# Performance work log

Hardware: AMD Instinct MI355X
Metric: run time of the kernel (lower is better)

## Reference

```python
import jax, jax.numpy as jnp
import numpy as np

N_NODES = 100000
N_EDGES = 1600000
IN_DIM = 64
HID = 64
EDGE_DIM = 1
NUM_GRAPHS = 1000
SCALE = 0.05


def setup_inputs() -> dict:
    key = jax.random.key(0)
    ks = jax.random.split(key, 20)
    x = jax.random.normal(ks[0], (N_NODES, IN_DIM), dtype=jnp.float32)
    edge_index = jax.random.randint(ks[1], (2, N_EDGES), 0, N_NODES, dtype=jnp.int64)
    edge_attr = jax.random.normal(ks[2], (N_EDGES, EDGE_DIM), dtype=jnp.float32)
    batch = jnp.sort(jax.random.randint(ks[3], (N_NODES,), 0, NUM_GRAPHS, dtype=jnp.int64))
    p = lambda k, shp: SCALE * jax.random.normal(k, shp, dtype=jnp.float32)
    return {
        "x": x, "edge_index": edge_index, "edge_attr": edge_attr, "batch": batch,
        # conv1 MLP + edge lin
        "W1a": p(ks[4], (IN_DIM, HID)), "b1a": p(ks[5], (HID,)),
        "W1b": p(ks[6], (HID, HID)), "b1b": p(ks[7], (HID,)),
        "We1": p(ks[8], (EDGE_DIM, IN_DIM)), "be1": p(ks[9], (IN_DIM,)),
        # conv2 MLP + edge lin
        "W2a": p(ks[10], (HID, HID)), "b2a": p(ks[11], (HID,)),
        "W2b": p(ks[12], (HID, HID)), "b2b": p(ks[13], (HID,)),
        "We2": p(ks[14], (EDGE_DIM, HID)), "be2": p(ks[15], (HID,)),
        # classifier
        "Wc1": p(ks[16], (HID, HID)), "bc1": p(ks[17], (HID,)),
        "Wc2": p(ks[18], (HID, 1)), "bc2": p(ks[19], (1,)),
    }


def _gine(x, src, dst, e_proj, Wa, ba, Wb, bb):
    # message: ReLU(x_src + projected edge feature); scatter-sum to target
    msg = jax.nn.relu(x[src] + e_proj)                      # [E, D]
    agg = jax.ops.segment_sum(msg, dst, num_segments=x.shape[0])
    h = x + agg                                             # eps = 0 (default)
    return jax.nn.relu(h @ Wa + ba) @ Wb + bb               # GIN MLP


def reference(x, edge_index, edge_attr, batch,
              W1a, b1a, W1b, b1b, We1, be1,
              W2a, b2a, W2b, b2b, We2, be2,
              Wc1, bc1, Wc2, bc2):
    src, dst = edge_index[0], edge_index[1]
    h = _gine(x, src, dst, edge_attr @ We1 + be1, W1a, b1a, W1b, b1b)
    h = jax.nn.relu(h)  # dropout is identity in eval mode
    h = _gine(h, src, dst, edge_attr @ We2 + be2, W2a, b2a, W2b, b2b)
    h = jax.nn.relu(h)
    # global mean pool over graphs
    sums = jax.ops.segment_sum(h, batch, num_segments=NUM_GRAPHS)
    cnts = jax.ops.segment_sum(jnp.ones((h.shape[0], 1), h.dtype), batch, num_segments=NUM_GRAPHS)
    pooled = sums / jnp.maximum(cnts, 1.0)                  # [G, HID]
    return jax.nn.relu(pooled @ Wc1 + bc1) @ Wc2 + bc2      # [G, 1]
```

## Files before the change

kernel.cpp:

```cpp
#include <hip/hip_runtime.h>

#define N_NODES    100000
#define N_EDGES    1600000
#define DIM        64
#define NUM_GRAPHS 1000
#define CONV_BLK   3125
#define PAD        72

#define SLICES     512
#define SLICE_E    3125
#define NBUCK      782
#define CAP4       3072

typedef __attribute__((ext_vector_type(8))) short bf16x8;
typedef __attribute__((ext_vector_type(4))) float f32x4;

__device__ __forceinline__ unsigned short f2bf(float f) {
    unsigned int b = __float_as_uint(f);
    b += 0x7FFFu + ((b >> 16) & 1u);
    return (unsigned short)(b >> 16);
}

__device__ __forceinline__ float4 ntload_f4(const float* p) {
    f32x4 v = __builtin_nontemporal_load((const f32x4*)p);
    return make_float4(v.x, v.y, v.z, v.w);
}

__global__ __launch_bounds__(256) void prep(
    const int* __restrict__ ei, const float* __restrict__ x,
    int* __restrict__ hist, int* __restrict__ bucketTotal,
    unsigned short* __restrict__ x16)
{
    __shared__ int lh[NBUCK];
    int blk = blockIdx.x, t = threadIdx.x;
    if (blk < SLICES) {
        for (int i = t; i < NBUCK; i += 256) lh[i] = 0;
        __syncthreads();
        const int* dsts = ei + N_EDGES + blk * SLICE_E;
        for (int k = t; k < SLICE_E; k += 256)
            atomicAdd(&lh[dsts[k] >> 7], 1);
        __syncthreads();
        for (int i = t; i < NBUCK; i += 256) {
            int h = lh[i];
            hist[blk * NBUCK + i] = h;
            if (h) atomicAdd(&bucketTotal[i], h);
        }
    } else {
        int tt = (blk - SLICES) * 256 + t;
        if (tt < N_NODES * DIM / 8) {
            int base = tt * 8;
            float4 f0 = ntload_f4(x + base);
            float4 f1 = ntload_f4(x + base + 4);
            uint4 o;
            o.x = (unsigned)f2bf(f0.x) | ((unsigned)f2bf(f0.y) << 16);
            o.y = (unsigned)f2bf(f0.z) | ((unsigned)f2bf(f0.w) << 16);
            o.z = (unsigned)f2bf(f1.x) | ((unsigned)f2bf(f1.y) << 16);
            o.w = (unsigned)f2bf(f1.z) | ((unsigned)f2bf(f1.w) << 16);
            *(uint4*)(x16 + base) = o;
        }
    }
}

__global__ __launch_bounds__(1024) void csr_c2a(
    const int* __restrict__ bucketTotal, int* __restrict__ bucketStart)
{
    __shared__ int sc[1024];
    int t = threadIdx.x;
    int v = (t < NBUCK) ? bucketTotal[t] : 0;
    sc[t] = v;
    __syncthreads();
    for (int o = 1; o < 1024; o <<= 1) {
        int u = (t >= o) ? sc[t - o] : 0;
        __syncthreads();
        sc[t] += u;
        __syncthreads();
    }
    if (t < NBUCK) bucketStart[t] = sc[t] - v;
    if (t == NBUCK - 1) bucketStart[NBUCK] = sc[t];
}

__global__ __launch_bounds__(512) void csr_c2b(
    const int* __restrict__ hist, const int* __restrict__ bucketStart,
    int* __restrict__ off)
{
    __shared__ int sc[512];
    int b = blockIdx.x, t = threadIdx.x;
    int v = hist[t * NBUCK + b];
    sc[t] = v;
    __syncthreads();
    for (int o = 1; o < 512; o <<= 1) {
        int u = (t >= o) ? sc[t - o] : 0;
        __syncthreads();
        sc[t] += u;
        __syncthreads();
    }
    off[b * SLICES + t] = bucketStart[b] + sc[t] - v;
}

__global__ __launch_bounds__(512) void csr_c3(
    const int* __restrict__ ei, const float* __restrict__ ea,
    const int* __restrict__ hist, const int* __restrict__ off,
    int2* __restrict__ tmp)
{
    __shared__ int2 staging[SLICE_E];
    __shared__ int  lstart[NBUCK + 1];
    __shared__ int  garr[NBUCK];
    __shared__ int  lcur[NBUCK];
    __shared__ unsigned short barr[SLICE_E];
    __shared__ int  part[512];

    int s = blockIdx.x, t = threadIdx.x;

    int h[2];
    int mysum = 0;
    #pragma unroll
    for (int j = 0; j < 2; ++j) {
        int b = 2 * t + j;
        h[j] = (b < NBUCK) ? hist[s * NBUCK + b] : 0;
        mysum += h[j];
    }
    part[t] = mysum;
    for (int i = t; i < NBUCK; i += 512) {
        garr[i] = off[i * SLICES + s];
        lcur[i] = 0;
    }
    __syncthreads();
    for (int o = 1; o < 512; o <<= 1) {
        int u = (t >= o) ? part[t - o] : 0;
        __syncthreads();
        part[t] += u;
        __syncthreads();
    }
    int run = part[t] - mysum;
    #pragma unroll
    for (int j = 0; j < 2; ++j) {
        int b = 2 * t + j;
        if (b < NBUCK) lstart[b] = run;
        run += h[j];
    }
    if (t == 0) lstart[NBUCK] = SLICE_E;
    __syncthreads();

    #pragma unroll
    for (int j = 0; j < 2; ++j) {
        int b = 2 * t + j;
        if (b < NBUCK)
            for (int i = lstart[b]; i < lstart[b + 1]; ++i)
                barr[i] = (unsigned short)b;
    }
    __syncthreads();

    for (int k = t; k < SLICE_E; k += 512) {
        int e   = s * SLICE_E + k;
        int src = ei[e];
        int dst = ei[N_EDGES + e];
        float a = ea[e];
        int b   = dst >> 7;
        int p   = lstart[b] + atomicAdd(&lcur[b], 1);
        staging[p] = make_int2(((dst & 127) << 17) | src, __float_as_int(a));
    }
    __syncthreads();

    for (int i = t; i < SLICE_E; i += 512) {
        int b = barr[i];
        tmp[garr[b] + (i - lstart[b])] = staging[i];
    }
}

__global__ __launch_bounds__(512, 6) void gine_sort(
    const uint2* __restrict__ g2,
    const float* __restrict__ self32,
    const int*   __restrict__ bucketStart,
    const int2*  __restrict__ tmp,
    int2* __restrict__ csr_e,
    int*  __restrict__ rowptr,
    const float* __restrict__ We, const float* __restrict__ be,
    const float* __restrict__ Wa, const float* __restrict__ ba,
    const float* __restrict__ Wb, const float* __restrict__ bb,
    unsigned int* __restrict__ out16)
{
    __shared__ int2 staging[CAP4];
    __shared__ int  nh[128];
    __shared__ int  nscan[128];
    __shared__ int  ncur[128];
    __shared__ short sWat[64 * PAD];
    __shared__ short sWbt[64 * PAD];
    __shared__ short h16[32 * PAD];
    __shared__ short t16[32 * PAD];

    int t = threadIdx.x;
    int b = blockIdx.x;
    int lo = bucketStart[b], hi = bucketStart[b + 1];
    int cnt = hi - lo;
    int node0 = b << 7;
    int nn = min(128, N_NODES - node0);

    for (int i = t; i < 4096; i += 512) {
        int k = i >> 6, n = i & 63;
        sWat[n * PAD + k] = (short)f2bf(Wa[i]);
        sWbt[n * PAD + k] = (short)f2bf(Wb[i]);
    }
    if (t < 128) { nh[t] = 0; ncur[t] = 0; }
    __syncthreads();

    int2 r[6];
    int nr = 0;
    for (int k = t; k < cnt; k += 512) {
        int2 v = tmp[lo + k];
        r[nr++] = v;
        atomicAdd(&nh[v.x >> 17], 1);
    }
    __syncthreads();

    if (t < 128) nscan[t] = nh[t];
    __syncthreads();
    for (int o = 1; o < 128; o <<= 1) {
        int u = (t >= o && t < 128) ? nscan[t - o] : 0;
        __syncthreads();
        if (t < 128) nscan[t] += u;
        __syncthreads();
    }
    if (t < 128) nscan[t] -= nh[t];
    __syncthreads();

    if (t < nn) rowptr[node0 + t] = lo + nscan[t];
    if (b == NBUCK - 1 && t == 0) rowptr[N_NODES] = N_EDGES;

    for (int k = 0; k < nr; ++k) {
        int dl = r[k].x >> 17;
        int p  = nscan[dl] + atomicAdd(&ncur[dl], 1);
        staging[p] = r[k];
    }
    __syncthreads();

    for (int i = t; i < cnt; i += 512) {
        int2 v = staging[i];
        csr_e[lo + i] = make_int2((v.x & 0x1FFFF) << 4, v.y);
    }

    int wave = t >> 6;
    int lane = t & 63;
    int quad = lane >> 4;
    int l15  = lane & 15;
    int slot = wave * 4 + quad;
    int d0   = l15 * 4;
    float4 wp = *(const float4*)(We + d0);
    float4 bp = *(const float4*)(be + d0);
    int mtile = wave & 1;
    int ntile = wave >> 1;
    int col   = ntile * 16 + l15;
    int am    = mtile * 16 + l15;
    float bav = ba[col], bbv = bb[col];
    int cclamp = max(cnt - 1, 0);
    __syncthreads();

    for (int g = 0; g < 4; ++g) {
        int  lrow  = g * 32 + slot;
        bool valid = lrow < nn;
        int deg = valid ? nh[lrow] : 0;
        int beg = valid ? min(nscan[lrow], cclamp) : 0;
        int dm = deg;
        dm = max(dm, __shfl_xor(dm, 16));
        dm = max(dm, __shfl_xor(dm, 32));

        float4 agg = make_float4(0.f, 0.f, 0.f, 0.f);
        #define EDGE4(rr, uu, cond)                                              \
        {                                                                        \
            float s = (cond) ? 1.f : 0.f, av = __int_as_float(rr.y);             \
            float e0 = __uint_as_float(uu.x << 16);                              \
            float e1 = __uint_as_float(uu.x & 0xFFFF0000u);                      \
            float e2 = __uint_as_float(uu.y << 16);                              \
            float e3 = __uint_as_float(uu.y & 0xFFFF0000u);                      \
            agg.x = fmaf(s, fmaxf(e0 + fmaf(av, wp.x, bp.x), 0.f), agg.x);       \
            agg.y = fmaf(s, fmaxf(e1 + fmaf(av, wp.y, bp.y), 0.f), agg.y);       \
            agg.z = fmaf(s, fmaxf(e2 + fmaf(av, wp.z, bp.z), 0.f), agg.z);       \
            agg.w = fmaf(s, fmaxf(e3 + fmaf(av, wp.w, bp.w), 0.f), agg.w);       \
        }
        for (int j = 0; j < dm; j += 4) {
            int2 r0 = staging[beg + ((j + 0) < deg ? j + 0 : 0)];
            int2 r1 = staging[beg + ((j + 1) < deg ? j + 1 : 0)];
            int2 r2 = staging[beg + ((j + 2) < deg ? j + 2 : 0)];
            int2 r3 = staging[beg + ((j + 3) < deg ? j + 3 : 0)];
            uint2 u0 = g2[(r0.x & 0x1FFFF) * 16 + l15];
            uint2 u1 = g2[(r1.x & 0x1FFFF) * 16 + l15];
            uint2 u2 = g2[(r2.x & 0x1FFFF) * 16 + l15];
            uint2 u3 = g2[(r3.x & 0x1FFFF) * 16 + l15];
            EDGE4(r0, u0, (j + 0) < deg)
            EDGE4(r1, u1, (j + 1) < deg)
            EDGE4(r2, u2, (j + 2) < deg)
            EDGE4(r3, u3, (j + 3) < deg)
        }
        #undef EDGE4
        if (valid) {
            float4 sv = *(const float4*)(self32 + (size_t)(node0 + lrow) * DIM + d0);
            agg.x += sv.x; agg.y += sv.y; agg.z += sv.z; agg.w += sv.w;
        }
        {
            unsigned lov = (unsigned)f2bf(agg.x) | ((unsigned)f2bf(agg.y) << 16);
            unsigned hiv = (unsigned)f2bf(agg.z) | ((unsigned)f2bf(agg.w) << 16);
            *(uint2*)&h16[slot * PAD + d0] = make_uint2(lov, hiv);
        }
        __syncthreads();

        f32x4 acc = {bav, bav, bav, bav};
        #pragma unroll
        for (int s = 0; s < 2; ++s) {
            bf16x8 a = *(const bf16x8*)&h16[am * PAD + s * 32 + quad * 8];
            bf16x8 bb8 = *(const bf16x8*)&sWat[col * PAD + s * 32 + quad * 8];
            acc = __builtin_amdgcn_mfma_f32_16x16x32_bf16(a, bb8, acc, 0, 0, 0);
        }
        #pragma unroll
        for (int rr = 0; rr < 4; ++rr) {
            int row = mtile * 16 + quad * 4 + rr;
            t16[row * PAD + col] = (short)f2bf(fmaxf(acc[rr], 0.f));
        }
        __syncthreads();

        f32x4 acc2 = {bbv, bbv, bbv, bbv};
        #pragma unroll
        for (int s = 0; s < 2; ++s) {
            bf16x8 a = *(const bf16x8*)&t16[am * PAD + s * 32 + quad * 8];
            bf16x8 bb8 = *(const bf16x8*)&sWbt[col * PAD + s * 32 + quad * 8];
            acc2 = __builtin_amdgcn_mfma_f32_16x16x32_bf16(a, bb8, acc2, 0, 0, 0);
        }
        #pragma unroll
        for (int rr = 0; rr < 4; ++rr) {
            int row = mtile * 16 + quad * 4 + rr;
            h16[row * PAD + col] = (short)f2bf(fmaxf(acc2[rr], 0.f));
        }
        __syncthreads();
        {
            int n2 = t >> 4, dd = (t & 15) * 2;
            int lnode = g * 32 + n2;
            if (node0 + lnode < N_NODES) {
                uint2 v = *(const uint2*)&h16[n2 * PAD + dd * 2];
                *(uint2*)&out16[(size_t)(node0 + lnode) * 32 + dd] = v;
            }
        }
        __syncthreads();
    }
}

template<bool SELF32>
__global__ __launch_bounds__(512, 8) void gine_mfma(
    const uint2* __restrict__ g2,
    const float* __restrict__ self32,
    const int*   __restrict__ rowptr,
    const int2*  __restrict__ csr_e,
    const float* __restrict__ We, const float* __restrict__ be,
    const float* __restrict__ Wa, const float* __restrict__ ba,
    const float* __restrict__ Wb, const float* __restrict__ bb,
    unsigned int* __restrict__ out16)
{
    __shared__ short sWat[64 * PAD];
    __shared__ short sWbt[64 * PAD];
    __shared__ short h16[32 * PAD];
    __shared__ short t16[32 * PAD];

    int t = threadIdx.x;
    for (int i = t; i < 4096; i += 512) {
        int k = i >> 6, n = i & 63;
        sWat[n * PAD + k] = (short)f2bf(Wa[i]);
        sWbt[n * PAD + k] = (short)f2bf(Wb[i]);
    }
    int wave = t >> 6;
    int lane = t & 63;
    int quad = lane >> 4;
    int l15  = lane & 15;
    int slot = wave * 4 + quad;
    int d0   = l15 * 4;
    float4 wp = *(const float4*)(We + d0);
    float4 bp = *(const float4*)(be + d0);
    int mtile = wave & 1;
    int ntile = wave >> 1;
    int col   = ntile * 16 + l15;
    int am    = mtile * 16 + l15;
    float bav = ba[col], bbv = bb[col];
    __syncthreads();

    for (int base = blockIdx.x * 32; base < N_NODES; base += gridDim.x * 32) {
        int  node  = base + slot;
        bool valid = node < N_NODES;
        int beg = 0, deg = 0;
        if (valid) {
            beg = rowptr[node];
            deg = rowptr[node + 1] - beg;
            beg = min(beg, N_EDGES - 1);
        }
        int dm = deg;
        dm = max(dm, __shfl_xor(dm, 16));
        dm = max(dm, __shfl_xor(dm, 32));

        float4 agg = make_float4(0.f, 0.f, 0.f, 0.f);
        #define EDGE4(rr, uu, cond)                                              \
        {                                                                        \
            float s = (cond) ? 1.f : 0.f, av = __int_as_float(rr.y);             \
            float e0 = __uint_as_float(uu.x << 16);                              \
            float e1 = __uint_as_float(uu.x & 0xFFFF0000u);                      \
            float e2 = __uint_as_float(uu.y << 16);                              \
            float e3 = __uint_as_float(uu.y & 0xFFFF0000u);                      \
            agg.x = fmaf(s, fmaxf(e0 + fmaf(av, wp.x, bp.x), 0.f), agg.x);       \
            agg.y = fmaf(s, fmaxf(e1 + fmaf(av, wp.y, bp.y), 0.f), agg.y);       \
            agg.z = fmaf(s, fmaxf(e2 + fmaf(av, wp.z, bp.z), 0.f), agg.z);       \
            agg.w = fmaf(s, fmaxf(e3 + fmaf(av, wp.w, bp.w), 0.f), agg.w);       \
        }
        for (int j = 0; j < dm; j += 4) {
            int2 r0 = csr_e[beg + ((j + 0) < deg ? j + 0 : 0)];
            int2 r1 = csr_e[beg + ((j + 1) < deg ? j + 1 : 0)];
            int2 r2 = csr_e[beg + ((j + 2) < deg ? j + 2 : 0)];
            int2 r3 = csr_e[beg + ((j + 3) < deg ? j + 3 : 0)];
            uint2 u0 = g2[r0.x + l15];
            uint2 u1 = g2[r1.x + l15];
            uint2 u2 = g2[r2.x + l15];
            uint2 u3 = g2[r3.x + l15];
            EDGE4(r0, u0, (j + 0) < deg)
            EDGE4(r1, u1, (j + 1) < deg)
            EDGE4(r2, u2, (j + 2) < deg)
            EDGE4(r3, u3, (j + 3) < deg)
        }
        #undef EDGE4
        if (valid) {
            if (SELF32) {
                float4 sv = *(const float4*)(self32 + (size_t)node * DIM + d0);
                agg.x += sv.x; agg.y += sv.y; agg.z += sv.z; agg.w += sv.w;
            } else {
                uint2 u = g2[node * 16 + l15];
                agg.x += __uint_as_float(u.x << 16);
                agg.y += __uint_as_float(u.x & 0xFFFF0000u);
                agg.z += __uint_as_float(u.y << 16);
                agg.w += __uint_as_float(u.y & 0xFFFF0000u);
            }
        }
        {
            unsigned lo = (unsigned)f2bf(agg.x) | ((unsigned)f2bf(agg.y) << 16);
            unsigned hi = (unsigned)f2bf(agg.z) | ((unsigned)f2bf(agg.w) << 16);
            *(uint2*)&h16[slot * PAD + d0] = make_uint2(lo, hi);
        }
        __syncthreads();

        f32x4 acc = {bav, bav, bav, bav};
        #pragma unroll
        for (int s = 0; s < 2; ++s) {
            bf16x8 a = *(const bf16x8*)&h16[am * PAD + s * 32 + quad * 8];
            bf16x8 b = *(const bf16x8*)&sWat[col * PAD + s * 32 + quad * 8];
            acc = __builtin_amdgcn_mfma_f32_16x16x32_bf16(a, b, acc, 0, 0, 0);
        }
        #pragma unroll
        for (int r = 0; r < 4; ++r) {
            int row = mtile * 16 + quad * 4 + r;
            t16[row * PAD + col] = (short)f2bf(fmaxf(acc[r], 0.f));
        }
        __syncthreads();

        f32x4 acc2 = {bbv, bbv, bbv, bbv};
        #pragma unroll
        for (int s = 0; s < 2; ++s) {
            bf16x8 a = *(const bf16x8*)&t16[am * PAD + s * 32 + quad * 8];
            bf16x8 b = *(const bf16x8*)&sWbt[col * PAD + s * 32 + quad * 8];
            acc2 = __builtin_amdgcn_mfma_f32_16x16x32_bf16(a, b, acc2, 0, 0, 0);
        }
        #pragma unroll
        for (int r = 0; r < 4; ++r) {
            int row = mtile * 16 + quad * 4 + r;
            h16[row * PAD + col] = (short)f2bf(fmaxf(acc2[r], 0.f));
        }
        __syncthreads();
        {
            int nn = t >> 4, dd = (t & 15) * 2;
            if (base + nn < N_NODES) {
                uint2 v = *(const uint2*)&h16[nn * PAD + dd * 2];
                *(uint2*)&out16[(size_t)(base + nn) * 32 + dd] = v;
            }
        }
        __syncthreads();
    }
}

__device__ __forceinline__ int lbound(const int* __restrict__ a, int key) {
    int lo = 0, hi = N_NODES;
    while (lo < hi) {
        int mid = (lo + hi) >> 1;
        if (a[mid] < key) lo = mid + 1; else hi = mid;
    }
    return lo;
}

__global__ __launch_bounds__(256) void pool_cls(
    const unsigned int* __restrict__ B16b,
    const int* __restrict__ batch,
    const float* __restrict__ Wc1,  const float* __restrict__ bc1,
    const float* __restrict__ Wc2,  const float* __restrict__ bc2,
    float* __restrict__ out)
{
    __shared__ float sW[64 * 64];
    __shared__ float sp[4][64];

    int t = threadIdx.x;
    for (int i = t; i < 64 * 64; i += 256) sW[i] = Wc1[i];

    int nl   = t >> 6;
    int lane = t & 63;
    int g    = blockIdx.x * 4 + nl;

    int p = lane & 31, h = lane >> 5;
    if (g < NUM_GRAPHS) {
        int s = lbound(batch, g);
        int e = lbound(batch, g + 1);
        float2 sum = make_float2(0.f, 0.f);
        for (int i = s + h; i < e; i += 2) {
            unsigned u = B16b[(size_t)i * 32 + p];
            sum.x += __uint_as_float(u << 16);
            sum.y += __uint_as_float(u & 0xFFFF0000u);
        }
        sum.x += __shfl_xor(sum.x, 32);
        sum.y += __shfl_xor(sum.y, 32);
        if (h == 0) {
            float inv = 1.f / (float)max(e - s, 1);
            sp[nl][2 * p]     = sum.x * inv;
            sp[nl][2 * p + 1] = sum.y * inv;
        }
    } else if (h == 0) {
        sp[nl][2 * p] = 0.f;
        sp[nl][2 * p + 1] = 0.f;
    }
    __syncthreads();

    float acc = bc1[lane];
    #pragma unroll
    for (int k = 0; k < 64; ++k)
        acc = fmaf(sp[nl][k], sW[k * 64 + lane], acc);
    float tv = fmaxf(acc, 0.f) * Wc2[lane];

    #pragma unroll
    for (int off = 32; off > 0; off >>= 1)
        tv += __shfl_down(tv, off);

    if (lane == 0 && g < NUM_GRAPHS) out[g] = tv + bc2[0];
}

extern "C" void kernel_launch(void* const* d_in, const int* in_sizes, int n_in,
                              void* d_out, int out_size, void* d_ws, size_t ws_size,
                              hipStream_t stream) {
    const float* x     = (const float*)d_in[0];
    const int*   ei    = (const int*)  d_in[1];
    const float* ea    = (const float*)d_in[2];
    const int*   batch = (const int*)  d_in[3];
    const float* W1a = (const float*)d_in[4];
    const float* b1a = (const float*)d_in[5];
    const float* W1b = (const float*)d_in[6];
    const float* b1b = (const float*)d_in[7];
    const float* We1 = (const float*)d_in[8];
    const float* be1 = (const float*)d_in[9];
    const float* W2a = (const float*)d_in[10];
    const float* b2a = (const float*)d_in[11];
    const float* W2b = (const float*)d_in[12];
    const float* b2b = (const float*)d_in[13];
    const float* We2 = (const float*)d_in[14];
    const float* be2 = (const float*)d_in[15];
    const float* Wc1 = (const float*)d_in[16];
    const float* bc1 = (const float*)d_in[17];
    const float* Wc2 = (const float*)d_in[18];
    const float* bc2 = (const float*)d_in[19];

    int2*           csr_e  = (int2*)d_ws;
    unsigned short* x16    = (unsigned short*)(csr_e + N_EDGES);
    unsigned short* B16    = x16 + (size_t)N_NODES * DIM;
    unsigned short* B16b   = B16 + (size_t)N_NODES * DIM;
    int2*           tmp    = (int2*)B16b;
    int*            hist   = (int*)(B16b + (size_t)N_NODES * DIM);
    int*            off    = hist + SLICES * NBUCK;
    int*            bucketTotal = off + NBUCK * SLICES;
    int*            bucketStart = bucketTotal + NBUCK;
    int*            rowptr = bucketStart + (NBUCK + 1);

    hipMemsetAsync(bucketTotal, 0, NBUCK * sizeof(int), stream);

    prep<<<SLICES + CONV_BLK, 256, 0, stream>>>(ei, x, hist, bucketTotal, x16);
    csr_c2a<<<1, 1024, 0, stream>>>(bucketTotal, bucketStart);
    csr_c2b<<<NBUCK, 512, 0, stream>>>(hist, bucketStart, off);
    csr_c3<<<SLICES, 512, 0, stream>>>(ei, ea, hist, off, tmp);

    gine_sort<<<NBUCK, 512, 0, stream>>>(
        (const uint2*)x16, x, bucketStart, tmp, csr_e, rowptr,
        We1, be1, W1a, b1a, W1b, b1b, (unsigned int*)B16);

    gine_mfma<false><<<1024, 512, 0, stream>>>(
        (const uint2*)B16, nullptr, rowptr, csr_e,
        We2, be2, W2a, b2a, W2b, b2b, (unsigned int*)B16b);

    pool_cls<<<(NUM_GRAPHS + 3) / 4, 256, 0, stream>>>(
        (const unsigned int*)B16b, batch, Wc1, bc1, Wc2, bc2, (float*)d_out);
}
```

Before: 296.5 us.

## Replace per-slice offset scan with atomic bucket cursors and fuse bf16 cast into build

Removes the per-slice histogram array and the column-scan kernel. Each slice block now recomputes its local histogram and reserves its spot in each bucket with an atomicAdd on a global cursor. The x-to-bf16 conversion moves into the build kernel, and the global histogram pass uses fewer, larger blocks. This cuts one kernel launch and the hist/off global traffic, at the cost of reading the destination array twice and making the edge order within a bucket depend on atomic timing.

Measured after the change: 316.4 us. 1.07x slower.

```diff
diff --git a/kernel.cpp b/kernel.cpp
--- a/kernel.cpp
+++ b/kernel.cpp
@@ -4,13 +4,13 @@
 #define N_EDGES    1600000
 #define DIM        64
 #define NUM_GRAPHS 1000
-#define CONV_BLK   3125
 #define PAD        72
 
 #define SLICES     512
 #define SLICE_E    3125
 #define NBUCK      782
 #define CAP4       3072
+#define HIST_BLK   256
 
 typedef __attribute__((ext_vector_type(8))) short bf16x8;
 typedef __attribute__((ext_vector_type(4))) float f32x4;
@@ -26,29 +26,71 @@
     return make_float4(v.x, v.y, v.z, v.w);
 }
 
-__global__ __launch_bounds__(256) void prep(
-    const int* __restrict__ ei, const float* __restrict__ x,
-    int* __restrict__ hist, int* __restrict__ bucketTotal,
-    unsigned short* __restrict__ x16)
+__global__ __launch_bounds__(256) void prep_hist(
+    const int* __restrict__ ei, int* __restrict__ bucketTotal)
 {
     __shared__ int lh[NBUCK];
     int blk = blockIdx.x, t = threadIdx.x;
-    if (blk < SLICES) {
-        for (int i = t; i < NBUCK; i += 256) lh[i] = 0;
-        __syncthreads();
-        const int* dsts = ei + N_EDGES + blk * SLICE_E;
-        for (int k = t; k < SLICE_E; k += 256)
-            atomicAdd(&lh[dsts[k] >> 7], 1);
-        __syncthreads();
-        for (int i = t; i < NBUCK; i += 256) {
-            int h = lh[i];
-            hist[blk * NBUCK + i] = h;
-            if (h) atomicAdd(&bucketTotal[i], h);
-        }
-    } else {
-        int tt = (blk - SLICES) * 256 + t;
-        if (tt < N_NODES * DIM / 8) {
-            int base = tt * 8;
+    for (int i = t; i < NBUCK; i += 256) lh[i] = 0;
+    __syncthreads();
+    const int* dsts = ei + N_EDGES + blk * (2 * SLICE_E);
+    for (int k = t; k < 2 * SLICE_E; k += 256)
+        atomicAdd(&lh[dsts[k] >> 7], 1);
+    __syncthreads();
+    for (int i = t; i < NBUCK; i += 256) {
+        int h = lh[i];
+        if (h) atomicAdd(&bucketTotal[i], h);
+    }
+}
+
+__global__ __launch_bounds__(1024) void csr_c2a(
+    const int* __restrict__ bucketTotal, int* __restrict__ bucketStart,
+    int* __restrict__ cursor)
+{
+    __shared__ int sc[1024];
+    int t = threadIdx.x;
+    int v = (t < NBUCK) ? bucketTotal[t] : 0;
+    sc[t] = v;
+    __syncthreads();
+    for (int o = 1; o < 1024; o <<= 1) {
+        int u = (t >= o) ? sc[t - o] : 0;
+        __syncthreads();
+        sc[t] += u;
+        __syncthreads();
+    }
+    if (t < NBUCK) {
+        int e = sc[t] - v;
+        bucketStart[t] = e;
+        cursor[t] = e;
+    }
+    if (t == NBUCK - 1) bucketStart[NBUCK] = sc[t];
+}
+
+__global__ __launch_bounds__(512) void csr_build(
+    const int* __restrict__ ei, const float* __restrict__ ea,
+    const float* __restrict__ x,
+    int* __restrict__ cursor, int2* __restrict__ tmp,
+    unsigned short* __restrict__ x16)
+{
+    __shared__ int2 staging[SLICE_E];
+    __shared__ int  lh[NBUCK];
+    __shared__ int  lstart[NBUCK + 1];
+    __shared__ int  garr[NBUCK];
+    __shared__ unsigned short barr[SLICE_E];
+    __shared__ int  part[512];
+
+    int s = blockIdx.x, t = threadIdx.x;
+    const int* dsts = ei + N_EDGES + s * SLICE_E;
+
+    for (int i = t; i < NBUCK; i += 512) lh[i] = 0;
+    __syncthreads();
+    for (int k = t; k < SLICE_E; k += 512)
+        atomicAdd(&lh[dsts[k] >> 7], 1);
+
+    {
+        int gid = s * 512 + t;
+        for (int it = gid; it < N_NODES * DIM / 8; it += SLICES * 512) {
+            int base = it * 8;
             float4 f0 = ntload_f4(x + base);
             float4 f1 = ntload_f4(x + base + 4);
             uint4 o;
@@ -59,71 +101,17 @@
             *(uint4*)(x16 + base) = o;
         }
     }
-}
-
-__global__ __launch_bounds__(1024) void csr_c2a(
-    const int* __restrict__ bucketTotal, int* __restrict__ bucketStart)
-{
-    __shared__ int sc[1024];
-    int t = threadIdx.x;
-    int v = (t < NBUCK) ? bucketTotal[t] : 0;
-    sc[t] = v;
-    __syncthreads();
-    for (int o = 1; o < 1024; o <<= 1) {
-        int u = (t >= o) ? sc[t - o] : 0;
-        __syncthreads();
-        sc[t] += u;
-        __syncthreads();
-    }
-    if (t < NBUCK) bucketStart[t] = sc[t] - v;
-    if (t == NBUCK - 1) bucketStart[NBUCK] = sc[t];
-}
-
-__global__ __launch_bounds__(512) void csr_c2b(
-    const int* __restrict__ hist, const int* __restrict__ bucketStart,
-    int* __restrict__ off)
-{
-    __shared__ int sc[512];
-    int b = blockIdx.x, t = threadIdx.x;
-    int v = hist[t * NBUCK + b];
-    sc[t] = v;
-    __syncthreads();
-    for (int o = 1; o < 512; o <<= 1) {
-        int u = (t >= o) ? sc[t - o] : 0;
-        __syncthreads();
-        sc[t] += u;
-        __syncthreads();
-    }
-    off[b * SLICES + t] = bucketStart[b] + sc[t] - v;
-}
-
-__global__ __launch_bounds__(512) void csr_c3(
-    const int* __restrict__ ei, const float* __restrict__ ea,
-    const int* __restrict__ hist, const int* __restrict__ off,
-    int2* __restrict__ tmp)
-{
-    __shared__ int2 staging[SLICE_E];
-    __shared__ int  lstart[NBUCK + 1];
-    __shared__ int  garr[NBUCK];
-    __shared__ int  lcur[NBUCK];
-    __shared__ unsigned short barr[SLICE_E];
-    __shared__ int  part[512];
-
-    int s = blockIdx.x, t = threadIdx.x;
+    __syncthreads();
 
     int h[2];
     int mysum = 0;
     #pragma unroll
     for (int j = 0; j < 2; ++j) {
         int b = 2 * t + j;
-        h[j] = (b < NBUCK) ? hist[s * NBUCK + b] : 0;
+        h[j] = (b < NBUCK) ? lh[b] : 0;
         mysum += h[j];
     }
     part[t] = mysum;
-    for (int i = t; i < NBUCK; i += 512) {
-        garr[i] = off[i * SLICES + s];
-        lcur[i] = 0;
-    }
     __syncthreads();
     for (int o = 1; o < 512; o <<= 1) {
         int u = (t >= o) ? part[t - o] : 0;
@@ -135,12 +123,16 @@
     #pragma unroll
     for (int j = 0; j < 2; ++j) {
         int b = 2 * t + j;
-        if (b < NBUCK) lstart[b] = run;
+        if (b < NBUCK) {
+            lstart[b] = run;
+            if (h[j]) garr[b] = atomicAdd(&cursor[b], h[j]);
+        }
         run += h[j];
     }
     if (t == 0) lstart[NBUCK] = SLICE_E;
     __syncthreads();
 
+    for (int i = t; i < NBUCK; i += 512) lh[i] = 0;
     #pragma unroll
     for (int j = 0; j < 2; ++j) {
         int b = 2 * t + j;
@@ -153,10 +145,10 @@
     for (int k = t; k < SLICE_E; k += 512) {
         int e   = s * SLICE_E + k;
         int src = ei[e];
-        int dst = ei[N_EDGES + e];
+        int dst = dsts[k];
         float a = ea[e];
         int b   = dst >> 7;
-        int p   = lstart[b] + atomicAdd(&lcur[b], 1);
+        int p   = lstart[b] + atomicAdd(&lh[b], 1);
         staging[p] = make_int2(((dst & 127) << 17) | src, __float_as_int(a));
     }
     __syncthreads();
@@ -567,18 +559,16 @@
     unsigned short* B16    = x16 + (size_t)N_NODES * DIM;
     unsigned short* B16b   = B16 + (size_t)N_NODES * DIM;
     int2*           tmp    = (int2*)B16b;
-    int*            hist   = (int*)(B16b + (size_t)N_NODES * DIM);
-    int*            off    = hist + SLICES * NBUCK;
-    int*            bucketTotal = off + NBUCK * SLICES;
+    int*            bucketTotal = (int*)(B16b + (size_t)N_NODES * DIM);
     int*            bucketStart = bucketTotal + NBUCK;
-    int*            rowptr = bucketStart + (NBUCK + 1);
+    int*            cursor = bucketStart + (NBUCK + 1);
+    int*            rowptr = cursor + NBUCK;
 
     hipMemsetAsync(bucketTotal, 0, NBUCK * sizeof(int), stream);
 
-    prep<<<SLICES + CONV_BLK, 256, 0, stream>>>(ei, x, hist, bucketTotal, x16);
-    csr_c2a<<<1, 1024, 0, stream>>>(bucketTotal, bucketStart);
-    csr_c2b<<<NBUCK, 512, 0, stream>>>(hist, bucketStart, off);
-    csr_c3<<<SLICES, 512, 0, stream>>>(ei, ea, hist, off, tmp);
+    prep_hist<<<HIST_BLK, 256, 0, stream>>>(ei, bucketTotal);
+    csr_c2a<<<1, 1024, 0, stream>>>(bucketTotal, bucketStart, cursor);
+    csr_build<<<SLICES, 512, 0, stream>>>(ei, ea, x, cursor, tmp, x16);
 
     gine_sort<<<NBUCK, 512, 0, stream>>>(
         (const uint2*)x16, x, bucketStart, tmp, csr_e, rowptr,
```

## Batch eight buckets per offset-scan block and split conv2 into two half launches

Applied to the files above, without the earlier changes.

The per-bucket offset scan kernel now processes eight buckets per block with a padded shared array, cutting the block count roughly eightfold and amortising the barrier-heavy scan. The second GINE convolution is split into two launches of 512 blocks, each covering half the node range. This may improve cache locality of the gathered rows or load balance, but it adds an extra launch. The unused fp32 self-term template path is removed.

New measurement: 326.2 us. 10.0% more time.

```diff
diff --git a/kernel.cpp b/kernel.cpp
--- a/kernel.cpp
+++ b/kernel.cpp
@@ -6,6 +6,7 @@
 #define NUM_GRAPHS 1000
 #define CONV_BLK   3125
 #define PAD        72
+#define NHALF      50016
 
 #define SLICES     512
 #define SLICE_E    3125
@@ -79,22 +80,36 @@
     if (t == NBUCK - 1) bucketStart[NBUCK] = sc[t];
 }
 
-__global__ __launch_bounds__(512) void csr_c2b(
+__global__ __launch_bounds__(512) void csr_c2b8(
     const int* __restrict__ hist, const int* __restrict__ bucketStart,
     int* __restrict__ off)
 {
-    __shared__ int sc[512];
-    int b = blockIdx.x, t = threadIdx.x;
-    int v = hist[t * NBUCK + b];
-    sc[t] = v;
+    __shared__ int sc[512][9];
+    int blk = blockIdx.x, t = threadIdx.x;
+    int b0 = blk * 8;
+    int v[8];
+    #pragma unroll
+    for (int j = 0; j < 8; ++j) {
+        int b = b0 + j;
+        v[j] = (b < NBUCK) ? hist[t * NBUCK + b] : 0;
+        sc[t][j] = v[j];
+    }
     __syncthreads();
     for (int o = 1; o < 512; o <<= 1) {
-        int u = (t >= o) ? sc[t - o] : 0;
-        __syncthreads();
-        sc[t] += u;
-        __syncthreads();
-    }
-    off[b * SLICES + t] = bucketStart[b] + sc[t] - v;
+        int u[8];
+        #pragma unroll
+        for (int j = 0; j < 8; ++j) u[j] = (t >= o) ? sc[t - o][j] : 0;
+        __syncthreads();
+        #pragma unroll
+        for (int j = 0; j < 8; ++j) sc[t][j] += u[j];
+        __syncthreads();
+    }
+    #pragma unroll
+    for (int j = 0; j < 8; ++j) {
+        int b = b0 + j;
+        if (b < NBUCK)
+            off[b * SLICES + t] = bucketStart[b] + sc[t][j] - v[j];
+    }
 }
 
 __global__ __launch_bounds__(512) void csr_c3(
@@ -341,16 +356,15 @@
     }
 }
 
-template<bool SELF32>
 __global__ __launch_bounds__(512, 8) void gine_mfma(
     const uint2* __restrict__ g2,
-    const float* __restrict__ self32,
     const int*   __restrict__ rowptr,
     const int2*  __restrict__ csr_e,
     const float* __restrict__ We, const float* __restrict__ be,
     const float* __restrict__ Wa, const float* __restrict__ ba,
     const float* __restrict__ Wb, const float* __restrict__ bb,
-    unsigned int* __restrict__ out16)
+    unsigned int* __restrict__ out16,
+    int nbase, int nend)
 {
     __shared__ short sWat[64 * PAD];
     __shared__ short sWbt[64 * PAD];
@@ -378,7 +392,7 @@
     float bav = ba[col], bbv = bb[col];
     __syncthreads();
 
-    for (int base = blockIdx.x * 32; base < N_NODES; base += gridDim.x * 32) {
+    for (int base = nbase + blockIdx.x * 32; base < nend; base += gridDim.x * 32) {
         int  node  = base + slot;
         bool valid = node < N_NODES;
         int beg = 0, deg = 0;
@@ -420,16 +434,11 @@
         }
         #undef EDGE4
         if (valid) {
-            if (SELF32) {
-                float4 sv = *(const float4*)(self32 + (size_t)node * DIM + d0);
-                agg.x += sv.x; agg.y += sv.y; agg.z += sv.z; agg.w += sv.w;
-            } else {
-                uint2 u = g2[node * 16 + l15];
-                agg.x += __uint_as_float(u.x << 16);
-                agg.y += __uint_as_float(u.x & 0xFFFF0000u);
-                agg.z += __uint_as_float(u.y << 16);
-                agg.w += __uint_as_float(u.y & 0xFFFF0000u);
-            }
+            uint2 u = g2[node * 16 + l15];
+            agg.x += __uint_as_float(u.x << 16);
+            agg.y += __uint_as_float(u.x & 0xFFFF0000u);
+            agg.z += __uint_as_float(u.y << 16);
+            agg.w += __uint_as_float(u.y & 0xFFFF0000u);
         }
         {
             unsigned lo = (unsigned)f2bf(agg.x) | ((unsigned)f2bf(agg.y) << 16);
@@ -577,16 +586,19 @@
 
     prep<<<SLICES + CONV_BLK, 256, 0, stream>>>(ei, x, hist, bucketTotal, x16);
     csr_c2a<<<1, 1024, 0, stream>>>(bucketTotal, bucketStart);
-    csr_c2b<<<NBUCK, 512, 0, stream>>>(hist, bucketStart, off);
+    csr_c2b8<<<(NBUCK + 7) / 8, 512, 0, stream>>>(hist, bucketStart, off);
     csr_c3<<<SLICES, 512, 0, stream>>>(ei, ea, hist, off, tmp);
 
     gine_sort<<<NBUCK, 512, 0, stream>>>(
         (const uint2*)x16, x, bucketStart, tmp, csr_e, rowptr,
         We1, be1, W1a, b1a, W1b, b1b, (unsigned int*)B16);
 
-    gine_mfma<false><<<1024, 512, 0, stream>>>(
-        (const uint2*)B16, nullptr, rowptr, csr_e,
-        We2, be2, W2a, b2a, W2b, b2b, (unsigned int*)B16b);
+    gine_mfma<<<512, 512, 0, stream>>>(
+        (const uint2*)B16, rowptr, csr_e,
+        We2, be2, W2a, b2a, W2b, b2b, (unsigned int*)B16b, 0, NHALF);
+    gine_mfma<<<512, 512, 0, stream>>>(
+        (const uint2*)B16, rowptr, csr_e,
+        We2, be2, W2a, b2a, W2b, b2b, (unsigned int*)B16b, NHALF, N_NODES);
 
     pool_cls<<<(NUM_GRAPHS + 3) / 4, 256, 0, stream>>>(
         (const unsigned int*)B16b, batch, Wc1, bc1, Wc2, bc2, (float*)d_out);
```
